# Performance work log

Hardware: AMD Instinct MI355X
Metric: run time of the kernel (lower is better)

## Reference

```python
import jax, jax.numpy as jnp
import numpy as np


def setup_inputs() -> dict:
    key = jax.random.key(0)
    k1, k2, k3 = jax.random.split(key, 3)
    N, C, H, W, S = 9, 32, 192, 256, 9  # 1 ref + 8 src views, 3x3 patch samples
    f = jax.random.normal(k1, (N, C, H, W, S), dtype=jnp.float32)
    Wp = jax.random.normal(k2, (C, C), dtype=jnp.float32) / np.sqrt(C)  # Conv1d(C,C,1) weight
    bp = jax.random.normal(k3, (C,), dtype=jnp.float32) * 0.01  # Conv1d bias
    return {"f": f, "Wp": Wp, "bp": bp, "o": 2, "G": 8}


def reference(f, Wp, bp, o, G):
    # f: (N, C, H, W, S); view 0 is the reference image, views 1..N-1 are sources.
    N, C, H, W, S = f.shape
    ref = f[0]          # (C, H, W, S)
    src = f[1:]         # (N-1, C, H, W, S)

    # 1x1 Conv1d projection of the reference patches (per-position linear).
    proj = jnp.einsum('dc,chws->dhws', Wp, ref) + bp[:, None, None, None]  # (C,H,W,S)

    # Dot-product attention of the center sample (S//2) against all S samples.
    logits = jnp.sum(proj[:, :, :, S // 2, None] * proj, axis=0) / jnp.sqrt(jnp.float32(C))  # (H,W,S)
    att = jax.nn.softmax(logits, axis=-1)  # (H,W,S)

    # Grouped correlation: split channels into G groups of Cg, dot within each group.
    Cg = C // G
    ref_g = ref.reshape(G, Cg, H, W, S)
    src_g = src.reshape(N - 1, G, Cg, H, W, S)
    gc = jnp.einsum('gchws,ngchws->nghws', ref_g, src_g)  # (N-1, G, H, W, S)

    # Attention-weighted reduction over the S patch-sample axis.
    return jnp.sum(gc * att[None, None], axis=-1)  # (N-1, G, H, W)
```

## Files before the change

kernel.cpp:

```cpp
#include <hip/hip_runtime.h>
#include <math.h>

#define NSRC 8
#define CCH  32
#define HH   192
#define WW   256
#define SS   9
#define GG   8

#define F_SC (HH*WW*SS)
#define F_SH (WW*SS)
#define F_SN (CCH*HH*WW*SS)

#define WS_M   0
#define WS_V   1024
#define WS_BB  1056

#define TILE_W  32
#define ROW_F   (TILE_W * SS)
#define TILE_F  (CCH * ROW_F)
#define QPT     9

__global__ void k0_precompute(const float* __restrict__ Wp,
                              const float* __restrict__ bp,
                              float* __restrict__ ws) {
    const float inv_sqrtC = 0.17677669529663687f;
    int t = threadIdx.x;
    for (int idx = t; idx < 1024; idx += 256) {
        int c = idx >> 5, c2 = idx & 31;
        float acc = 0.f;
        for (int d = 0; d < 32; ++d) acc = fmaf(Wp[d*32 + c], Wp[d*32 + c2], acc);
        ws[WS_M + idx] = acc * inv_sqrtC;
    }
    if (t < 32) {
        float acc = 0.f;
        for (int d = 0; d < 32; ++d) acc = fmaf(Wp[d*32 + t], bp[d], acc);
        ws[WS_V + t] = acc * inv_sqrtC;
    }
    if (t == 0) {
        float acc = 0.f;
        for (int d = 0; d < 32; ++d) acc = fmaf(bp[d], bp[d], acc);
        ws[WS_BB] = acc * inv_sqrtC;
    }
}

__global__ __launch_bounds__(256) void k_fused(const float* __restrict__ f,
                                               const float* __restrict__ ws,
                                               float* __restrict__ out) {
    __shared__ float buf[TILE_F];
    __shared__ float M_s[1024];
    __shared__ float v_s[32];
    __shared__ float bb_s;
    __shared__ float lgp[32 * 73];
    __shared__ float att_s[32 * SS];

    const int t  = threadIdx.x;
    const int wi = t & 31;
    const int j  = t >> 5;
    const int wv = t >> 6;
    const int w0 = blockIdx.x * TILE_W;
    const int h  = blockIdx.y;
    const long rowbase = (long)h * F_SH + (long)w0 * SS;

    ((float4*)M_s)[t] = ((const float4*)(ws + WS_M))[t];
    if (t < 32) v_s[t] = ws[WS_V + t];
    if (t == 0) bb_s = ws[WS_BB];

    auto stage = [&](const float* fr) {
        #pragma unroll
        for (int i = 0; i < QPT; ++i) {
            int q = i * 256 + t;
            int c = q / 72;
            int k = q - c * 72;
            const float* g = fr + (long)c * F_SC + rowbase + 4 * k;
            float* l = buf + (i * 1024 + wv * 256);
            __builtin_amdgcn_global_load_lds(
                (const __attribute__((address_space(1))) void*)g,
                (__attribute__((address_space(3))) void*)l,
                16, 0, 0);
        }
    };

    stage(f);
    __syncthreads();

    float rref[4 * SS];
    #pragma unroll
    for (int cc = 0; cc < 4; ++cc) {
        const int c = 4 * j + cc;
        #pragma unroll
        for (int s = 0; s < SS; ++s)
            rref[cc * SS + s] = buf[c * ROW_F + wi * SS + s];
    }

    float u[4];
    #pragma unroll
    for (int cc = 0; cc < 4; ++cc) u[cc] = v_s[4 * j + cc];
    #pragma unroll
    for (int cp = 0; cp < 32; ++cp) {
        float r4 = buf[cp * ROW_F + wi * SS + 4];
        #pragma unroll
        for (int cc = 0; cc < 4; ++cc)
            u[cc] = fmaf(M_s[(4 * j + cc) * 32 + cp], r4, u[cc]);
    }

    float pb = 0.f;
    #pragma unroll
    for (int cc = 0; cc < 4; ++cc) pb = fmaf(rref[cc * SS + 4], v_s[4 * j + cc], pb);

    float lgv[SS];
    #pragma unroll
    for (int s = 0; s < SS; ++s) lgv[s] = pb;
    #pragma unroll
    for (int cc = 0; cc < 4; ++cc) {
        float uc = u[cc];
        #pragma unroll
        for (int s = 0; s < SS; ++s) lgv[s] = fmaf(uc, rref[cc * SS + s], lgv[s]);
    }
    #pragma unroll
    for (int s = 0; s < SS; ++s) lgp[wi * 73 + j * SS + s] = lgv[s];
    __syncthreads();

    if (j == 0) {
        float lt[SS];
        #pragma unroll
        for (int s = 0; s < SS; ++s) lt[s] = bb_s;
        #pragma unroll
        for (int jj = 0; jj < 8; ++jj)
            #pragma unroll
            for (int s = 0; s < SS; ++s) lt[s] += lgp[wi * 73 + jj * SS + s];
        float m = lt[0];
        #pragma unroll
        for (int s = 1; s < SS; ++s) m = fmaxf(m, lt[s]);
        float e[SS], sum = 0.f;
        #pragma unroll
        for (int s = 0; s < SS; ++s) { e[s] = __expf(lt[s] - m); sum += e[s]; }
        float inv = 1.f / sum;
        #pragma unroll
        for (int s = 0; s < SS; ++s) att_s[wi * SS + s] = e[s] * inv;
    }
    stage(f + (long)1 * F_SN);
    __syncthreads();

    float a[SS];
    #pragma unroll
    for (int s = 0; s < SS; ++s) a[s] = att_s[wi * SS + s];
    float qv[4 * SS];
    #pragma unroll
    for (int cc = 0; cc < 4; ++cc)
        #pragma unroll
        for (int s = 0; s < SS; ++s)
            qv[cc * SS + s] = a[s] * rref[cc * SS + s];

    #pragma unroll 1
    for (int n = 0; n < NSRC; ++n) {
        float acc = 0.f;
        #pragma unroll
        for (int cc = 0; cc < 4; ++cc) {
            const int c = 4 * j + cc;
            #pragma unroll
            for (int s = 0; s < SS; ++s)
                acc = fmaf(qv[cc * SS + s], buf[c * ROW_F + wi * SS + s], acc);
        }
        out[(((long)n * GG + j) * HH + h) * WW + w0 + wi] = acc;
        if (n < NSRC - 1) {
            __syncthreads();
            stage(f + (long)(n + 2) * F_SN);
            __syncthreads();
        }
    }
}

extern "C" void kernel_launch(void* const* d_in, const int* in_sizes, int n_in,
                              void* d_out, int out_size, void* d_ws, size_t ws_size,
                              hipStream_t stream) {
    const float* f  = (const float*)d_in[0];
    const float* Wp = (const float*)d_in[1];
    const float* bp = (const float*)d_in[2];
    float* out = (float*)d_out;
    float* ws  = (float*)d_ws;

    k0_precompute<<<1, 256, 0, stream>>>(Wp, bp, ws);
    k_fused<<<dim3(WW / TILE_W, HH), 256, 0, stream>>>(f, ws, out);
}
```

Before: 660.9 us.

## Replace LDS staging with direct register loads double-buffered across source views

Drops the shared-memory tile staging through global_load_lds and the per-view __syncthreads barriers. Each thread now loads its own 4 channels × 9 samples straight into registers, using two alternating register buffers so the next view's loads are issued before the current view's correlation runs. This removes the block-wide syncs and LDS traffic, and the accumulation is split across four partial sums. In exchange each thread reads 36 floats with a stride of 9 floats between lanes, so global coalescing is weaker than the previous 16-byte vector copies, and register pressure rises.

```diff
diff --git a/kernel.cpp b/kernel.cpp
--- a/kernel.cpp
+++ b/kernel.cpp
@@ -16,10 +16,7 @@
 #define WS_V   1024
 #define WS_BB  1056
 
-#define TILE_W  32
-#define ROW_F   (TILE_W * SS)
-#define TILE_F  (CCH * ROW_F)
-#define QPT     9
+#define TILE_W 32
 
 __global__ void k0_precompute(const float* __restrict__ Wp,
                               const float* __restrict__ bp,
@@ -44,61 +41,71 @@
     }
 }
 
+
+#define LOADF(ARR, frame) do {                                                \
+    _Pragma("unroll")                                                         \
+    for (int cc = 0; cc < 4; ++cc) {                                          \
+        const float* p_ = fr + (long)(frame) * F_SN + (long)cc * F_SC;        \
+        _Pragma("unroll")                                                     \
+        for (int s = 0; s < SS; ++s) ARR[cc*SS + s] = p_[s];                  \
+    }                                                                         \
+} while (0)
+
+#define CORR_STORE(ARR, n) do {                                               \
+    float a0_ = 0.f, a1_ = 0.f, a2_ = 0.f, a3_ = 0.f;                         \
+    _Pragma("unroll")                                                         \
+    for (int s = 0; s < SS; ++s) {                                            \
+        a0_ = fmaf(rref[0*SS + s], ARR[0*SS + s], a0_);                       \
+        a1_ = fmaf(rref[1*SS + s], ARR[1*SS + s], a1_);                       \
+        a2_ = fmaf(rref[2*SS + s], ARR[2*SS + s], a2_);                       \
+        a3_ = fmaf(rref[3*SS + s], ARR[3*SS + s], a3_);                       \
+    }                                                                         \
+    out[(((long)(n) * GG + j) * HH + h) * WW + w0 + wi] = (a0_ + a1_) + (a2_ + a3_); \
+} while (0)
+
 __global__ __launch_bounds__(256) void k_fused(const float* __restrict__ f,
                                                const float* __restrict__ ws,
                                                float* __restrict__ out) {
-    __shared__ float buf[TILE_F];
     __shared__ float M_s[1024];
     __shared__ float v_s[32];
     __shared__ float bb_s;
+    __shared__ float s4[32 * 33];
     __shared__ float lgp[32 * 73];
     __shared__ float att_s[32 * SS];
 
     const int t  = threadIdx.x;
     const int wi = t & 31;
     const int j  = t >> 5;
-    const int wv = t >> 6;
     const int w0 = blockIdx.x * TILE_W;
     const int h  = blockIdx.y;
-    const long rowbase = (long)h * F_SH + (long)w0 * SS;
+    const float* fr = f + (long)(4 * j) * F_SC + (long)h * F_SH + (long)(w0 + wi) * SS;
 
     ((float4*)M_s)[t] = ((const float4*)(ws + WS_M))[t];
     if (t < 32) v_s[t] = ws[WS_V + t];
     if (t == 0) bb_s = ws[WS_BB];
 
-    auto stage = [&](const float* fr) {
-        #pragma unroll
-        for (int i = 0; i < QPT; ++i) {
-            int q = i * 256 + t;
-            int c = q / 72;
-            int k = q - c * 72;
-            const float* g = fr + (long)c * F_SC + rowbase + 4 * k;
-            float* l = buf + (i * 1024 + wv * 256);
-            __builtin_amdgcn_global_load_lds(
-                (const __attribute__((address_space(1))) void*)g,
-                (__attribute__((address_space(3))) void*)l,
-                16, 0, 0);
-        }
-    };
-
-    stage(f);
-    __syncthreads();
-
     float rref[4 * SS];
     #pragma unroll
     for (int cc = 0; cc < 4; ++cc) {
-        const int c = 4 * j + cc;
+        const float* p_ = fr + (long)cc * F_SC;
         #pragma unroll
-        for (int s = 0; s < SS; ++s)
-            rref[cc * SS + s] = buf[c * ROW_F + wi * SS + s];
+        for (int s = 0; s < SS; ++s) rref[cc*SS + s] = p_[s];
     }
+
+    float A[4 * SS], B[4 * SS];
+    LOADF(A, 1);
+
+    #pragma unroll
+    for (int cc = 0; cc < 4; ++cc)
+        s4[wi * 33 + 4 * j + cc] = rref[cc * SS + 4];
+    __syncthreads();
 
     float u[4];
     #pragma unroll
     for (int cc = 0; cc < 4; ++cc) u[cc] = v_s[4 * j + cc];
     #pragma unroll
     for (int cp = 0; cp < 32; ++cp) {
-        float r4 = buf[cp * ROW_F + wi * SS + 4];
+        float r4 = s4[wi * 33 + cp];
         #pragma unroll
         for (int cc = 0; cc < 4; ++cc)
             u[cc] = fmaf(M_s[(4 * j + cc) * 32 + cp], r4, u[cc]);
@@ -139,35 +146,25 @@
         #pragma unroll
         for (int s = 0; s < SS; ++s) att_s[wi * SS + s] = e[s] * inv;
     }
-    stage(f + (long)1 * F_SN);
     __syncthreads();
 
-    float a[SS];
-    #pragma unroll
-    for (int s = 0; s < SS; ++s) a[s] = att_s[wi * SS + s];
-    float qv[4 * SS];
-    #pragma unroll
-    for (int cc = 0; cc < 4; ++cc)
+    {
+        float a[SS];
         #pragma unroll
-        for (int s = 0; s < SS; ++s)
-            qv[cc * SS + s] = a[s] * rref[cc * SS + s];
-
-    #pragma unroll 1
-    for (int n = 0; n < NSRC; ++n) {
-        float acc = 0.f;
+        for (int s = 0; s < SS; ++s) a[s] = att_s[wi * SS + s];
         #pragma unroll
-        for (int cc = 0; cc < 4; ++cc) {
-            const int c = 4 * j + cc;
+        for (int cc = 0; cc < 4; ++cc)
             #pragma unroll
             for (int s = 0; s < SS; ++s)
-                acc = fmaf(qv[cc * SS + s], buf[c * ROW_F + wi * SS + s], acc);
-        }
-        out[(((long)n * GG + j) * HH + h) * WW + w0 + wi] = acc;
-        if (n < NSRC - 1) {
-            __syncthreads();
-            stage(f + (long)(n + 2) * F_SN);
-            __syncthreads();
-        }
+                rref[cc * SS + s] *= a[s];
+    }
+
+    #pragma unroll
+    for (int n = 0; n < NSRC; n += 2) {
+        LOADF(B, n + 2);
+        CORR_STORE(A, n);
+        if (n + 2 < NSRC) LOADF(A, n + 3);
+        CORR_STORE(B, n + 1);
     }
 }
 
```

Result: no change. 661.7 us (+0.1%).
